# Kernel optimization log

Hardware: AMD Instinct MI355X
Metric: run time of the kernel (lower is better)

## Reference

```python
import jax, jax.numpy as jnp
import numpy as np

B = 131072          # batch of fermion configurations
S = 256             # sys_size
NUP = 16            # num_fillings[0]
NDOWN = 16          # num_fillings[1]


def _random_occupancy(rng, b, s, nfill):
    # exactly `nfill` ones per row, uniformly random positions
    r = rng.random((b, s))
    perm_rank = np.argsort(r, axis=1).argsort(axis=1)  # a random permutation per row
    return (perm_rank < nfill).astype(np.float32)


def setup_inputs() -> dict:
    rng = np.random.default_rng(0)
    cfg_up = _random_occupancy(rng, B, S, NUP)
    cfg_down = _random_occupancy(rng, B, S, NDOWN)
    config_fermion = jnp.asarray(np.concatenate([cfg_up, cfg_down], axis=1))  # (B, 2S)
    key = jax.random.key(0)
    k1, k2 = jax.random.split(key)
    states_up = jax.random.normal(k1, (S, NUP), dtype=jnp.float32)
    states_down = jax.random.normal(k2, (S, NDOWN), dtype=jnp.float32)
    return {"config_fermion": config_fermion, "states_up": states_up, "states_down": states_down}


def reference(config_fermion, states_up, states_down):
    s = states_up.shape[0]
    nup = states_up.shape[1]
    ndown = states_down.shape[1]
    cfg_up = config_fermion[:, :s]      # (B, S) of {0,1}
    cfg_down = config_fermion[:, s:]
    # indices of occupied sites, ascending (torch.nonzero order); top_k breaks
    # ties by lowest index, then sort ascending
    idx_up = jnp.sort(jax.lax.top_k(cfg_up, nup)[1], axis=1)        # (B, Nup)
    idx_down = jnp.sort(jax.lax.top_k(cfg_down, ndown)[1], axis=1)  # (B, Ndown)
    mats_up = states_up[idx_up]         # (B, Nup, Nup) gather of orbital rows
    mats_down = states_down[idx_down]   # (B, Ndown, Ndown)
    det_up = jnp.linalg.det(mats_up)
    det_down = jnp.linalg.det(mats_down)
    return det_up * det_down
```

## Files before the change

### kernel.cpp

```cpp
#include <hip/hip_runtime.h>

static __device__ __forceinline__ unsigned umax2(unsigned a, unsigned b) { return a > b ? a : b; }

__global__ __launch_bounds__(256) void slater_det_main(
    const float* __restrict__ cfg,
    const float* __restrict__ sup,
    const float* __restrict__ sdn,
    float* __restrict__ out,
    unsigned* __restrict__ ws_count,
    unsigned* __restrict__ ws_rec,
    unsigned cap)
{
    __shared__ __align__(16) int idx_lds[4][16][16];

    const int tid  = threadIdx.x;
    const int wave = tid >> 6;
    const int lane = tid & 63;
    const int wb0  = (blockIdx.x * 4 + wave) * 8;

    float4 c[16];
#pragma unroll
    for (int d = 0; d < 16; ++d) {
        const float* p = cfg + (size_t)(wb0 + (d >> 1)) * 512
                             + (size_t)(d & 1) * 256 + (size_t)lane * 4;
        c[d] = *(const float4*)p;
    }
    const unsigned long long lt = (1ull << lane) - 1ull;
#pragma unroll
    for (int d = 0; d < 16; ++d) {
        float4 v = c[d];
        bool n0 = v.x != 0.f, n1 = v.y != 0.f, n2 = v.z != 0.f, n3 = v.w != 0.f;
        unsigned long long b0 = __ballot(n0);
        unsigned long long b1 = __ballot(n1);
        unsigned long long b2 = __ballot(n2);
        unsigned long long b3 = __ballot(n3);
        int base = __popcll(b0 & lt) + __popcll(b1 & lt)
                 + __popcll(b2 & lt) + __popcll(b3 & lt);
        int pos = lane * 4;
        int r = base;
        if (n0 && r < 16) idx_lds[wave][d][r] = pos;
        r += n0;
        if (n1 && r < 16) idx_lds[wave][d][r] = pos + 1;
        r += n1;
        if (n2 && r < 16) idx_lds[wave][d][r] = pos + 2;
        r += n2;
        if (n3 && r < 16) idx_lds[wave][d][r] = pos + 3;
    }
    __syncthreads();

    const int g = lane >> 2;
    const int q = lane & 3;
    const int4 ri = *(const int4*)&idx_lds[wave][g][q * 4];
    const float* tab = (g & 1) ? sdn : sup;
    const int rid[4] = {ri.x, ri.y, ri.z, ri.w};

    float rr[4][16];
#pragma unroll
    for (int j = 0; j < 4; ++j) {
        const float* p = tab + (size_t)rid[j] * 16;
        float4 a = *(const float4*)(p + 0);
        float4 b = *(const float4*)(p + 4);
        float4 e = *(const float4*)(p + 8);
        float4 f = *(const float4*)(p + 12);
        rr[j][0]=a.x;  rr[j][1]=a.y;  rr[j][2]=a.z;  rr[j][3]=a.w;
        rr[j][4]=b.x;  rr[j][5]=b.y;  rr[j][6]=b.z;  rr[j][7]=b.w;
        rr[j][8]=e.x;  rr[j][9]=e.y;  rr[j][10]=e.z; rr[j][11]=e.w;
        rr[j][12]=f.x; rr[j][13]=f.y; rr[j][14]=f.z; rr[j][15]=f.w;
    }

    const int gbase = lane & ~3;
    float det = 1.f;
    bool bad = false;
#pragma unroll
    for (int k = 0; k < 16; ++k) {
        const int src = gbase | (k >> 2);
        const int jp  = k & 3;
        float piv = __shfl(rr[jp][k], src);
        det *= piv;
        bad = bad || (fabsf(piv) < 1e-4f);
        float inv = __builtin_amdgcn_rcpf(piv);
        float f0 = rr[0][k] * inv;
        float f1 = rr[1][k] * inv;
        float f2 = rr[2][k] * inv;
        float f3 = rr[3][k] * inv;
#pragma unroll
        for (int cc = k + 1; cc < 16; ++cc) {
            float pcc = __shfl(rr[jp][cc], src);
            rr[0][cc] = __builtin_fmaf(-f0, pcc, rr[0][cc]);
            rr[1][cc] = __builtin_fmaf(-f1, pcc, rr[1][cc]);
            rr[2][cc] = __builtin_fmaf(-f2, pcc, rr[2][cc]);
            rr[3][cc] = __builtin_fmaf(-f3, pcc, rr[3][cc]);
        }
    }

    int badflag = bad ? 1 : 0;
    int partnerbad = __shfl_xor(badflag, 4);
    if ((badflag | partnerbad) && (lane & 7) == 0) {
        unsigned slot = atomicAdd(ws_count, 1u);
        if (slot < cap) {
            unsigned* rec = ws_rec + slot * 12;
            rec[0] = (unsigned)(wb0 + (lane >> 3));
            const int gU = lane >> 2;
#pragma unroll
            for (int t = 0; t < 4; ++t) {
                const int* iu = &idx_lds[wave][gU][t * 4];
                const int* id = &idx_lds[wave][gU | 1][t * 4];
                rec[1 + t] = (unsigned)iu[0] | ((unsigned)iu[1] << 8)
                           | ((unsigned)iu[2] << 16) | ((unsigned)iu[3] << 24);
                rec[5 + t] = (unsigned)id[0] | ((unsigned)id[1] << 8)
                           | ((unsigned)id[2] << 16) | ((unsigned)id[3] << 24);
            }
        }
    }

    float prod = det * __shfl_xor(det, 4);
    if ((lane & 7) == 0) out[wb0 + (lane >> 3)] = prod;
}

__global__ __launch_bounds__(256) void slater_det_cleanup(
    const float* __restrict__ sup,
    const float* __restrict__ sdn,
    float* __restrict__ out,
    const unsigned* __restrict__ ws_count,
    const unsigned* __restrict__ ws_rec,
    unsigned cap)
{
    unsigned n = *ws_count;
    if (n > cap) n = cap;
    const int tid  = blockIdx.x * 256 + threadIdx.x;
    const int unit = tid >> 3;
    const int nunits = (int)(gridDim.x * 256) >> 3;
    const int l8   = threadIdx.x & 7;
    const int wl   = threadIdx.x & 63;
    const int q    = wl & 3;
    const int gbase = wl & ~3;

    for (unsigned item = unit; item < n; item += nunits) {
        const unsigned* rec = ws_rec + item * 12;
        const unsigned batch = rec[0];
        const int half = l8 >> 2;
        const unsigned pk = rec[1 + half * 4 + q];
        const int rid[4] = { (int)(pk & 255u), (int)((pk >> 8) & 255u),
                             (int)((pk >> 16) & 255u), (int)(pk >> 24) };
        const float* tab = half ? sdn : sup;

        float rr[4][16];
#pragma unroll
        for (int j = 0; j < 4; ++j) {
            const float* p = tab + (size_t)rid[j] * 16;
            float4 a = *(const float4*)(p + 0);
            float4 b = *(const float4*)(p + 4);
            float4 e = *(const float4*)(p + 8);
            float4 f = *(const float4*)(p + 12);
            rr[j][0]=a.x;  rr[j][1]=a.y;  rr[j][2]=a.z;  rr[j][3]=a.w;
            rr[j][4]=b.x;  rr[j][5]=b.y;  rr[j][6]=b.z;  rr[j][7]=b.w;
            rr[j][8]=e.x;  rr[j][9]=e.y;  rr[j][10]=e.z; rr[j][11]=e.w;
            rr[j][12]=f.x; rr[j][13]=f.y; rr[j][14]=f.z; rr[j][15]=f.w;
        }

        unsigned am = 0xFu;
        float fdet = 1.f;
        int flips = 0;
#pragma unroll
        for (int k = 0; k < 16; ++k) {
            unsigned a0 = (__float_as_uint(rr[0][k]) & 0x7FFFFFF0u) | (unsigned)(q*4+0);
            unsigned a1 = (__float_as_uint(rr[1][k]) & 0x7FFFFFF0u) | (unsigned)(q*4+1);
            unsigned a2 = (__float_as_uint(rr[2][k]) & 0x7FFFFFF0u) | (unsigned)(q*4+2);
            unsigned a3 = (__float_as_uint(rr[3][k]) & 0x7FFFFFF0u) | (unsigned)(q*4+3);
            unsigned key0 = (am & 1u) ? a0 : (unsigned)(q*4+0);
            unsigned key1 = (am & 2u) ? a1 : (unsigned)(q*4+1);
            unsigned key2 = (am & 4u) ? a2 : (unsigned)(q*4+2);
            unsigned key3 = (am & 8u) ? a3 : (unsigned)(q*4+3);
            unsigned kloc = umax2(umax2(key0, key1), umax2(key2, key3));
            int jloc = (int)(kloc & 3u);
            float crow[16];
#pragma unroll
            for (int cc = k; cc < 16; ++cc) {
                float t01 = (jloc & 1) ? rr[1][cc] : rr[0][cc];
                float t23 = (jloc & 1) ? rr[3][cc] : rr[2][cc];
                crow[cc] = (jloc & 2) ? t23 : t01;
            }
            unsigned ko = kloc;
            ko = umax2(ko, (unsigned)__shfl_xor((int)ko, 1));
            ko = umax2(ko, (unsigned)__shfl_xor((int)ko, 2));
            int p   = (int)(ko & 15u);
            int src = gbase | (p >> 2);
            float prow[16];
#pragma unroll
            for (int cc = k; cc < 16; ++cc) prow[cc] = __shfl(crow[cc], src);
            float piv = prow[k];
            fdet *= piv;
            int t = p - q * 4;
            unsigned mlt = (t <= 0) ? 0u : ((t >= 4) ? 0xFu : ((1u << t) - 1u));
            int cnt = __popc(am & mlt);
            cnt += __shfl_xor(cnt, 1);
            cnt += __shfl_xor(cnt, 2);
            flips += cnt;
            if (q == (p >> 2)) am &= ~(1u << (p & 3));
            float inv = 1.0f / piv;
            float f0 = rr[0][k] * inv;
            float f1 = rr[1][k] * inv;
            float f2 = rr[2][k] * inv;
            float f3 = rr[3][k] * inv;
#pragma unroll
            for (int cc = k + 1; cc < 16; ++cc) {
                rr[0][cc] = __builtin_fmaf(-f0, prow[cc], rr[0][cc]);
                rr[1][cc] = __builtin_fmaf(-f1, prow[cc], rr[1][cc]);
                rr[2][cc] = __builtin_fmaf(-f2, prow[cc], rr[2][cc]);
                rr[3][cc] = __builtin_fmaf(-f3, prow[cc], rr[3][cc]);
            }
        }
        float det = (flips & 1) ? -fdet : fdet;
        float prod = det * __shfl_xor(det, 4);
        if (l8 == 0) out[batch] = prod;
    }
}

extern "C" void kernel_launch(void* const* d_in, const int* in_sizes, int n_in,
                              void* d_out, int out_size, void* d_ws, size_t ws_size,
                              hipStream_t stream) {
    const float* cfg = (const float*)d_in[0];
    const float* sup = (const float*)d_in[1];
    const float* sdn = (const float*)d_in[2];
    float* outp = (float*)d_out;
    unsigned* ws_count = (unsigned*)d_ws;
    unsigned* ws_rec   = (unsigned*)d_ws + 4;
    unsigned cap = (unsigned)((ws_size - 16) / 48);
    const int B = in_sizes[0] / 512;
    const int blocks = B / 32;

    hipMemsetAsync(d_ws, 0, 16, stream);
    slater_det_main<<<blocks, 256, 0, stream>>>(cfg, sup, sdn, outp,
                                                ws_count, ws_rec, cap);
    slater_det_cleanup<<<16, 256, 0, stream>>>(sup, sdn, outp,
                                               ws_count, ws_rec, cap);
}
```

Before: 67.81 us.

## Make main kernel persistent with prefetch of next chunk's configuration

Launches a fixed grid of 1024 blocks where each wave loops over 8-row chunks in grid-stride order, issuing the global loads for the next chunk's configuration before running elimination on the current one. This aims to hide config-load latency behind the determinant arithmetic and to cut block launch overhead. It keeps 64 extra VGPRs of prefetched data live during elimination, which may reduce occupancy, and replaces the block barrier with a wave-local LDS wait.

```diff
diff --git a/kernel.cpp b/kernel.cpp
--- a/kernel.cpp
+++ b/kernel.cpp
@@ -9,112 +9,135 @@
     float* __restrict__ out,
     unsigned* __restrict__ ws_count,
     unsigned* __restrict__ ws_rec,
-    unsigned cap)
+    unsigned cap,
+    int nchunks)
 {
     __shared__ __align__(16) int idx_lds[4][16][16];
 
     const int tid  = threadIdx.x;
     const int wave = tid >> 6;
     const int lane = tid & 63;
-    const int wb0  = (blockIdx.x * 4 + wave) * 8;
+    const int wgid = blockIdx.x * 4 + wave;
+    const int nw   = gridDim.x * 4;
+
+    const unsigned long long lt = (1ull << lane) - 1ull;
+    const int g = lane >> 2;
+    const int q = lane & 3;
+    const int gbase = lane & ~3;
+    const float* tab = (g & 1) ? sdn : sup;
 
     float4 c[16];
+    int cur = wgid;
+    if (cur >= nchunks) return;
+
 #pragma unroll
     for (int d = 0; d < 16; ++d) {
-        const float* p = cfg + (size_t)(wb0 + (d >> 1)) * 512
-                             + (size_t)(d & 1) * 256 + (size_t)lane * 4;
+        const float* p = cfg + (size_t)cur * 4096 + (size_t)d * 256 + (size_t)lane * 4;
         c[d] = *(const float4*)p;
     }
-    const unsigned long long lt = (1ull << lane) - 1ull;
-#pragma unroll
-    for (int d = 0; d < 16; ++d) {
-        float4 v = c[d];
-        bool n0 = v.x != 0.f, n1 = v.y != 0.f, n2 = v.z != 0.f, n3 = v.w != 0.f;
-        unsigned long long b0 = __ballot(n0);
-        unsigned long long b1 = __ballot(n1);
-        unsigned long long b2 = __ballot(n2);
-        unsigned long long b3 = __ballot(n3);
-        int base = __popcll(b0 & lt) + __popcll(b1 & lt)
-                 + __popcll(b2 & lt) + __popcll(b3 & lt);
-        int pos = lane * 4;
-        int r = base;
-        if (n0 && r < 16) idx_lds[wave][d][r] = pos;
-        r += n0;
-        if (n1 && r < 16) idx_lds[wave][d][r] = pos + 1;
-        r += n1;
-        if (n2 && r < 16) idx_lds[wave][d][r] = pos + 2;
-        r += n2;
-        if (n3 && r < 16) idx_lds[wave][d][r] = pos + 3;
+
+    while (cur < nchunks) {
+        const int nxt = cur + nw;
+
+#pragma unroll
+        for (int d = 0; d < 16; ++d) {
+            float4 v = c[d];
+            bool n0 = v.x != 0.f, n1 = v.y != 0.f, n2 = v.z != 0.f, n3 = v.w != 0.f;
+            unsigned long long b0 = __ballot(n0);
+            unsigned long long b1 = __ballot(n1);
+            unsigned long long b2 = __ballot(n2);
+            unsigned long long b3 = __ballot(n3);
+            int base = __popcll(b0 & lt) + __popcll(b1 & lt)
+                     + __popcll(b2 & lt) + __popcll(b3 & lt);
+            int pos = lane * 4;
+            int r = base;
+            if (n0 && r < 16) idx_lds[wave][d][r] = pos;
+            r += n0;
+            if (n1 && r < 16) idx_lds[wave][d][r] = pos + 1;
+            r += n1;
+            if (n2 && r < 16) idx_lds[wave][d][r] = pos + 2;
+            r += n2;
+            if (n3 && r < 16) idx_lds[wave][d][r] = pos + 3;
+        }
+        asm volatile("s_waitcnt lgkmcnt(0)" ::: "memory");
+        __builtin_amdgcn_sched_barrier(0);
+
+        const int4 ri = *(const int4*)&idx_lds[wave][g][q * 4];
+        const int rid[4] = {ri.x, ri.y, ri.z, ri.w};
+
+        float rr[4][16];
+#pragma unroll
+        for (int j = 0; j < 4; ++j) {
+            const float* p = tab + (size_t)rid[j] * 16;
+            float4 a = *(const float4*)(p + 0);
+            float4 b = *(const float4*)(p + 4);
+            float4 e = *(const float4*)(p + 8);
+            float4 f = *(const float4*)(p + 12);
+            rr[j][0]=a.x;  rr[j][1]=a.y;  rr[j][2]=a.z;  rr[j][3]=a.w;
+            rr[j][4]=b.x;  rr[j][5]=b.y;  rr[j][6]=b.z;  rr[j][7]=b.w;
+            rr[j][8]=e.x;  rr[j][9]=e.y;  rr[j][10]=e.z; rr[j][11]=e.w;
+            rr[j][12]=f.x; rr[j][13]=f.y; rr[j][14]=f.z; rr[j][15]=f.w;
+        }
+        __builtin_amdgcn_sched_barrier(0);
+
+        if (nxt < nchunks) {
+#pragma unroll
+            for (int d = 0; d < 16; ++d) {
+                const float* p = cfg + (size_t)nxt * 4096 + (size_t)d * 256 + (size_t)lane * 4;
+                c[d] = *(const float4*)p;
+            }
+        }
+        __builtin_amdgcn_sched_barrier(0);
+
+        float det = 1.f;
+        bool bad = false;
+#pragma unroll
+        for (int k = 0; k < 16; ++k) {
+            const int src = gbase | (k >> 2);
+            const int jp  = k & 3;
+            float piv = __shfl(rr[jp][k], src);
+            det *= piv;
+            bad = bad || (fabsf(piv) < 1e-4f);
+            float inv = __builtin_amdgcn_rcpf(piv);
+            float f0 = rr[0][k] * inv;
+            float f1 = rr[1][k] * inv;
+            float f2 = rr[2][k] * inv;
+            float f3 = rr[3][k] * inv;
+#pragma unroll
+            for (int cc = k + 1; cc < 16; ++cc) {
+                float pcc = __shfl(rr[jp][cc], src);
+                rr[0][cc] = __builtin_fmaf(-f0, pcc, rr[0][cc]);
+                rr[1][cc] = __builtin_fmaf(-f1, pcc, rr[1][cc]);
+                rr[2][cc] = __builtin_fmaf(-f2, pcc, rr[2][cc]);
+                rr[3][cc] = __builtin_fmaf(-f3, pcc, rr[3][cc]);
+            }
+        }
+
+        int badflag = bad ? 1 : 0;
+        int partnerbad = __shfl_xor(badflag, 4);
+        if ((badflag | partnerbad) && (lane & 7) == 0) {
+            unsigned slot = atomicAdd(ws_count, 1u);
+            if (slot < cap) {
+                unsigned* rec = ws_rec + slot * 12;
+                rec[0] = (unsigned)(cur * 8 + (lane >> 3));
+                const int gU = lane >> 2;
+#pragma unroll
+                for (int t = 0; t < 4; ++t) {
+                    const int* iu = &idx_lds[wave][gU][t * 4];
+                    const int* id = &idx_lds[wave][gU | 1][t * 4];
+                    rec[1 + t] = (unsigned)iu[0] | ((unsigned)iu[1] << 8)
+                               | ((unsigned)iu[2] << 16) | ((unsigned)iu[3] << 24);
+                    rec[5 + t] = (unsigned)id[0] | ((unsigned)id[1] << 8)
+                               | ((unsigned)id[2] << 16) | ((unsigned)id[3] << 24);
+                }
+            }
+        }
+
+        float prod = det * __shfl_xor(det, 4);
+        if ((lane & 7) == 0) out[cur * 8 + (lane >> 3)] = prod;
+
+        cur = nxt;
     }
-    __syncthreads();
-
-    const int g = lane >> 2;
-    const int q = lane & 3;
-    const int4 ri = *(const int4*)&idx_lds[wave][g][q * 4];
-    const float* tab = (g & 1) ? sdn : sup;
-    const int rid[4] = {ri.x, ri.y, ri.z, ri.w};
-
-    float rr[4][16];
-#pragma unroll
-    for (int j = 0; j < 4; ++j) {
-        const float* p = tab + (size_t)rid[j] * 16;
-        float4 a = *(const float4*)(p + 0);
-        float4 b = *(const float4*)(p + 4);
-        float4 e = *(const float4*)(p + 8);
-        float4 f = *(const float4*)(p + 12);
-        rr[j][0]=a.x;  rr[j][1]=a.y;  rr[j][2]=a.z;  rr[j][3]=a.w;
-        rr[j][4]=b.x;  rr[j][5]=b.y;  rr[j][6]=b.z;  rr[j][7]=b.w;
-        rr[j][8]=e.x;  rr[j][9]=e.y;  rr[j][10]=e.z; rr[j][11]=e.w;
-        rr[j][12]=f.x; rr[j][13]=f.y; rr[j][14]=f.z; rr[j][15]=f.w;
-    }
-
-    const int gbase = lane & ~3;
-    float det = 1.f;
-    bool bad = false;
-#pragma unroll
-    for (int k = 0; k < 16; ++k) {
-        const int src = gbase | (k >> 2);
-        const int jp  = k & 3;
-        float piv = __shfl(rr[jp][k], src);
-        det *= piv;
-        bad = bad || (fabsf(piv) < 1e-4f);
-        float inv = __builtin_amdgcn_rcpf(piv);
-        float f0 = rr[0][k] * inv;
-        float f1 = rr[1][k] * inv;
-        float f2 = rr[2][k] * inv;
-        float f3 = rr[3][k] * inv;
-#pragma unroll
-        for (int cc = k + 1; cc < 16; ++cc) {
-            float pcc = __shfl(rr[jp][cc], src);
-            rr[0][cc] = __builtin_fmaf(-f0, pcc, rr[0][cc]);
-            rr[1][cc] = __builtin_fmaf(-f1, pcc, rr[1][cc]);
-            rr[2][cc] = __builtin_fmaf(-f2, pcc, rr[2][cc]);
-            rr[3][cc] = __builtin_fmaf(-f3, pcc, rr[3][cc]);
-        }
-    }
-
-    int badflag = bad ? 1 : 0;
-    int partnerbad = __shfl_xor(badflag, 4);
-    if ((badflag | partnerbad) && (lane & 7) == 0) {
-        unsigned slot = atomicAdd(ws_count, 1u);
-        if (slot < cap) {
-            unsigned* rec = ws_rec + slot * 12;
-            rec[0] = (unsigned)(wb0 + (lane >> 3));
-            const int gU = lane >> 2;
-#pragma unroll
-            for (int t = 0; t < 4; ++t) {
-                const int* iu = &idx_lds[wave][gU][t * 4];
-                const int* id = &idx_lds[wave][gU | 1][t * 4];
-                rec[1 + t] = (unsigned)iu[0] | ((unsigned)iu[1] << 8)
-                           | ((unsigned)iu[2] << 16) | ((unsigned)iu[3] << 24);
-                rec[5 + t] = (unsigned)id[0] | ((unsigned)id[1] << 8)
-                           | ((unsigned)id[2] << 16) | ((unsigned)id[3] << 24);
-            }
-        }
-    }
-
-    float prod = det * __shfl_xor(det, 4);
-    if ((lane & 7) == 0) out[wb0 + (lane >> 3)] = prod;
 }
 
 __global__ __launch_bounds__(256) void slater_det_cleanup(
@@ -227,11 +250,11 @@
     unsigned* ws_rec   = (unsigned*)d_ws + 4;
     unsigned cap = (unsigned)((ws_size - 16) / 48);
     const int B = in_sizes[0] / 512;
-    const int blocks = B / 32;
+    const int nchunks = B / 8;
 
     hipMemsetAsync(d_ws, 0, 16, stream);
-    slater_det_main<<<blocks, 256, 0, stream>>>(cfg, sup, sdn, outp,
-                                                ws_count, ws_rec, cap);
+    slater_det_main<<<1024, 256, 0, stream>>>(cfg, sup, sdn, outp,
+                                              ws_count, ws_rec, cap, nchunks);
     slater_det_cleanup<<<16, 256, 0, stream>>>(sup, sdn, outp,
                                                ws_count, ws_rec, cap);
 }
```

After: 85.36 us. 1.26x slower.
